# Kernel tuning notes

Hardware: AMD Instinct MI355X
Metric: run time of the kernel (lower is better)

Reference implementation:

```python
import jax, jax.numpy as jnp
import numpy as np

H = 64   # gru_hidden_dim == gnn_hidden_dim
F = 64   # node_feat_dim
K = 8    # k_nn
OUT = 32 # output_factor_dim
BN_EPS = 1e-5


def _gru_scan(x, Wih, Whh, bih, bhh):
    # x: [S, F] single sequence (torch bug makes GRU scan the b*n axis); returns [S, H]
    xp = x @ Wih.T + bih  # [S, 3H], gate order r,z,n (torch convention)
    def step(h, xt):
        hp = h @ Whh.T + bhh
        r = jax.nn.sigmoid(xt[:H] + hp[:H])
        z = jax.nn.sigmoid(xt[H:2 * H] + hp[H:2 * H])
        ng = jnp.tanh(xt[2 * H:] + r * hp[2 * H:])
        hn = (1.0 - z) * ng + z * h
        return hn, hn
    _, out = jax.lax.scan(step, jnp.zeros((H,), x.dtype), xp)
    return out


def _gcn_layer(x, row, col, w, W, b, n):
    # PyG GCNConv: out[col] += d^{-1/2}[row] * w * d^{-1/2}[col] * (x @ W.T)[row] + b
    xw = x @ W.T
    deg = jnp.zeros((n,), x.dtype).at[col].add(w)
    dinv = deg ** -0.5
    dinv = jnp.where(jnp.isinf(dinv), 0.0, dinv)
    norm = dinv[row] * w * dinv[col]
    out = jnp.zeros_like(xw).at[col].add(norm[:, None] * xw[row])
    return out + b


def setup_inputs() -> dict:
    key = jax.random.key(0)
    ks = jax.random.split(key, 20)
    s = 0.08  # ~ torch uniform(-1/sqrt(64), 1/sqrt(64)) scale
    d = {
        'x_seq': jax.random.normal(ks[0], (4, 8, F, 2048), jnp.float32),
        # gru_sim params
        'Wih_s': jax.random.normal(ks[1], (3 * H, F), jnp.float32) * s,
        'Whh_s': jax.random.normal(ks[2], (3 * H, H), jnp.float32) * s,
        'bih_s': jax.random.normal(ks[3], (3 * H,), jnp.float32) * s,
        'bhh_s': jax.random.normal(ks[4], (3 * H,), jnp.float32) * s,
        # gru params
        'Wih': jax.random.normal(ks[5], (3 * H, F), jnp.float32) * s,
        'Whh': jax.random.normal(ks[6], (3 * H, H), jnp.float32) * s,
        'bih': jax.random.normal(ks[7], (3 * H,), jnp.float32) * s,
        'bhh': jax.random.normal(ks[8], (3 * H,), jnp.float32) * s,
        # gcn1 / gcn2 params (GCNConv weight [out,in], bias [out])
        'W1': jax.random.normal(ks[9], (H, H), jnp.float32) * s,
        'b1': jnp.zeros((H,), jnp.float32),
        'W2': jax.random.normal(ks[10], (H, H), jnp.float32) * s,
        'b2': jnp.zeros((H,), jnp.float32),
        # batchnorm affine
        'gamma': jnp.ones((H,), jnp.float32),
        'beta': jnp.zeros((H,), jnp.float32),
        # predictor
        'Wp': jax.random.normal(ks[11], (OUT, H), jnp.float32) * s,
        'bp': jnp.zeros((OUT,), jnp.float32),
    }
    return d


def reference(x_seq, Wih_s, Whh_s, bih_s, bhh_s, Wih, Whh, bih, bhh,
              W1, b1, W2, b2, gamma, beta, Wp, bp):
    b, l, f, n = x_seq.shape
    # torch GRU is batch_first=True but fed [l, b*n, f]: it scans the b*n axis
    # as time and gru_out[-1] keeps only batch item l-1 -> only last time slice used.
    seq = x_seq[:, -1].transpose(0, 2, 1).reshape(b * n, f)  # [b*n, f]
    h = _gru_scan(seq, Wih_s, Whh_s, bih_s, bhh_s).reshape(b, n, H)      # gru_sim
    h_out = _gru_scan(seq, Wih, Whh, bih, bhh).reshape(b, n, H)          # gru

    # dynamic kNN graph from similarity
    sim = jnp.einsum('bni,bmi->bnm', h, h)
    eye = jnp.eye(n, dtype=bool)
    sim = jnp.where(eye[None], jnp.asarray(-1e9, sim.dtype), sim)
    vals, idx = jax.lax.top_k(sim, K)  # [b, n, K], sorted desc like torch.topk

    # edges: n*K knn edges + n unit-weight self loops (outer add_self_loops;
    # GCNConv's add_remaining_self_loops then adds nothing)
    row = jnp.concatenate([jnp.repeat(jnp.arange(n), K), jnp.arange(n)])

    def per_graph(v, ix, x):
        col = jnp.concatenate([ix.reshape(-1), jnp.arange(n)])
        w = jnp.concatenate([v.reshape(-1), jnp.ones((n,), v.dtype)])
        o1 = jax.nn.relu(_gcn_layer(x, row, col, w, W1, b1, n))
        o2 = jax.nn.relu(_gcn_layer(o1, row, col, w, W2, b2, n))
        return o2

    out2 = jax.vmap(per_graph)(vals, idx, h_out)  # [b, n, H]

    # BatchNorm1d (training mode: biased batch stats over b*n rows)
    flat = out2.reshape(b * n, H)
    mu = flat.mean(0)
    var = flat.var(0)
    normed = (flat - mu) / jnp.sqrt(var + BN_EPS) * gamma + beta

    out = normed @ Wp.T + bp
    return out.reshape(b, n, OUT)
```

## Files before the change

kernel.cpp:

```cpp
#include <hip/hip_runtime.h>
#include <hip/hip_bf16.h>

typedef __hip_bfloat16 bf16;

#define NB   4
#define NN   2048
#define NROW 8192
#define HD   64
#define G3   192
#define KNN  8
#define OUTD 32
#define SCHUNK 32
#define SBURN  96
#define NCH    256
#define SCH4   32
#define SBRN4  40
#define NCH4   256
#define TI   4
#define TOPB 256
#define XPR  32
#define SCR  32
#define TKR  16

#define OFF_FLAG  0u
#define OFF_DEG   64u
#define OFF_DINV  8256u
#define OFF_BNS   16448u
#define OFF_BNSQ  16512u
#define OFF_SCALE 16576u
#define OFF_SHIFT 16640u
#define OFF_VALS  16704u
#define OFF_IDX   82240u
#define OFF_A     147776u
#define OFF_C     672064u
#define OFF_XP0   1196352u
#define OFF_XP1   2769216u
#define OFF_END   4342080u

typedef __attribute__((ext_vector_type(8))) short short8v;
typedef __attribute__((ext_vector_type(4))) float f32x4;

__device__ __forceinline__ float sigmoidf_(float x) { return 1.f / (1.f + __expf(-x)); }
__device__ __forceinline__ float tanhf_(float x) {
    float e = __expf(-2.f * fabsf(x));
    float t = (1.f - e) / (1.f + e);
    return copysignf(t, x);
}
__device__ __forceinline__ float ld(const void* p, size_t i, int isbf) {
    return isbf ? __bfloat162float(((const bf16*)p)[i]) : ((const float*)p)[i];
}
__device__ __forceinline__ float bcast(float v, int k) {
    return __int_as_float(__builtin_amdgcn_readlane(__float_as_int(v), k));
}
__device__ __forceinline__ unsigned short bf16rne(float f) {
    unsigned u = __float_as_uint(f);
    return (unsigned short)((u + 0x7FFFu + ((u >> 16) & 1u)) >> 16);
}

__global__ void probe_kernel(const void* __restrict__ gamma, int* __restrict__ flag)
{
    unsigned w = ((const unsigned*)gamma)[0];
    *flag = (w == 0x3F800000u) ? 0 : 1;
}

__global__ __launch_bounds__(384) void xp_kernel(
    const void* __restrict__ x_seq,
    const void* __restrict__ Wih_s, const void* __restrict__ bih_s,
    const void* __restrict__ Wih,   const void* __restrict__ bih,
    float* __restrict__ xp0, float* __restrict__ xp1,
    const int* __restrict__ dtp)
{
    int isbf = *dtp;
    int row0 = blockIdx.x * XPR;
    int b = row0 >> 11, j0 = row0 & 2047;
    int t = threadIdx.x;

    __shared__ __align__(16) float S[XPR * 68];
    for (int idx = t; idx < XPR * HD; idx += 384) {
        int f = idx >> 5, jj = idx & (XPR - 1);
        S[jj * 68 + f] = ld(x_seq, (size_t)((b * 8 + 7) * 64 + f) * 2048 + (j0 + jj), isbf);
    }

    int g = t % G3;
    const void* W  = (t < G3) ? Wih_s : Wih;
    const void* bi = (t < G3) ? bih_s : bih;
    float* o = (t < G3) ? xp0 : xp1;
    float wreg[64];
    #pragma unroll
    for (int k = 0; k < 64; ++k) wreg[k] = ld(W, g * HD + k, isbf);
    float bias = ld(bi, g, isbf);
    __syncthreads();

    for (int jj = 0; jj < XPR; ++jj) {
        const float4* s4 = (const float4*)(S + jj * 68);
        float a0 = bias, a1 = 0.f, a2 = 0.f, a3 = 0.f;
        #pragma unroll
        for (int q = 0; q < 16; ++q) {
            float4 v = s4[q];
            a0 += wreg[4*q+0] * v.x;
            a1 += wreg[4*q+1] * v.y;
            a2 += wreg[4*q+2] * v.z;
            a3 += wreg[4*q+3] * v.w;
        }
        o[(size_t)(row0 + jj) * G3 + g] = (a0 + a1) + (a2 + a3);
    }
}

__global__ __launch_bounds__(64) void gru_scan_pack_kernel(
    const float* __restrict__ xp0, const float* __restrict__ xp1,
    const void* __restrict__ Whh_s, const void* __restrict__ bhh_s,
    const void* __restrict__ Whh,   const void* __restrict__ bhh,
    unsigned short* __restrict__ hAhi, unsigned short* __restrict__ hAlo,
    float* __restrict__ hC,
    const int* __restrict__ dtp)
{
    int isbf = *dtp;
    int gru   = blockIdx.x >> 8;
    int chunk = blockIdx.x & (NCH4 - 1);
    const float* xpp = gru ? xp1 : xp0;
    const void* Wh   = gru ? Whh : Whh_s;
    const void* bh_p = gru ? bhh : bhh_s;

    int L = threadIdx.x;

    __shared__ __align__(16) float4 SW4[64 * 64];

    for (int k = 0; k < 64; ++k) {
        float4 v;
        v.x = ld(Wh, (size_t)L * 64 + k, isbf);
        v.y = ld(Wh, (size_t)(64 + L) * 64 + k, isbf);
        v.z = ld(Wh, (size_t)(128 + L) * 64 + k, isbf);
        v.w = 0.f;
        SW4[k * 64 + L] = v;
    }
    float br  = ld(bh_p, L, isbf);
    float bz  = ld(bh_p, 64 + L, isbf);
    float bn_ = ld(bh_p, 128 + L, isbf);
    __syncthreads();

    int first = chunk * SCH4;
    int burn  = min(SBRN4, first);
    int start = first - burn;
    int steps = burn + SCH4;

    float hval = 0.f;
    size_t rb = (size_t)start * G3;
    float xr = xpp[rb + L];
    float xz = xpp[rb + 64 + L];
    float xn = xpp[rb + 128 + L];

    for (int t = 0; t < steps; ++t) {
        size_t nb = (size_t)min(start + t + 1, NROW - 1) * G3;
        float pxr = xpp[nb + L];
        float pxz = xpp[nb + 64 + L];
        float pxn = xpp[nb + 128 + L];

        float pr0 = br, pz0 = bz, pn0 = bn_;
        float pr1 = 0.f, pz1 = 0.f, pn1 = 0.f;
        #pragma unroll
        for (int k = 0; k < 64; k += 2) {
            float4 w0 = SW4[k * 64 + L];
            float4 w1 = SW4[(k + 1) * 64 + L];
            float b0 = bcast(hval, k);
            float b1 = bcast(hval, k + 1);
            pr0 += w0.x * b0; pz0 += w0.y * b0; pn0 += w0.z * b0;
            pr1 += w1.x * b1; pz1 += w1.y * b1; pn1 += w1.z * b1;
        }

        float r  = sigmoidf_(xr + pr0 + pr1);
        float z  = sigmoidf_(xz + pz0 + pz1);
        float ng = tanhf_(xn + r * (pn0 + pn1));
        hval = (1.f - z) * ng + z * hval;

        if (t >= burn) {
            size_t o = (size_t)(start + t) * HD + L;
            if (gru) {
                hC[o] = hval;
            } else {
                unsigned short hb = bf16rne(hval);
                float hf = __uint_as_float(((unsigned)hb) << 16);
                hAhi[o] = hb;
                hAlo[o] = bf16rne(hval - hf);
            }
        }
        xr = pxr; xz = pxz; xn = pxn;
    }
}

__global__ __launch_bounds__(192, 2) void gru_scan_fused_kernel(
    const void* __restrict__ x_seq,
    const void* __restrict__ Wih_s, const void* __restrict__ bih_s,
    const void* __restrict__ Whh_s, const void* __restrict__ bhh_s,
    const void* __restrict__ Wih,   const void* __restrict__ bih,
    const void* __restrict__ Whh,   const void* __restrict__ bhh,
    float* __restrict__ hA, float* __restrict__ hC,
    const int* __restrict__ dtp)
{
    int isbf = *dtp;
    int gru   = blockIdx.x >> 8;
    int chunk = blockIdx.x & 255;
    const void* Wh = gru ? Whh : Whh_s;
    const void* bh_p = gru ? bhh : bhh_s;
    const void* Wi = gru ? Wih : Wih_s;
    const void* bi_p = gru ? bih : bih_s;
    float* hout = gru ? hC : hA;

    int lane = threadIdx.x & 63;
    int w    = threadIdx.x >> 6;
    int g    = w * 64 + lane;

    float whh[64], wih[64];
    #pragma unroll
    for (int k = 0; k < 64; ++k) {
        whh[k] = ld(Wh, g * 64 + k, isbf);
        wih[k] = ld(Wi, g * 64 + k, isbf);
    }
    float bh = ld(bh_p, g, isbf);
    float bi = ld(bi_p, g, isbf);

    __shared__ float hs[64];
    __shared__ float ss[64];
    __shared__ float gr[64], gz[64], ga[64], gx[64];

    int first = chunk * SCHUNK;
    int burn  = min(SBURN, first);
    int start = first - burn;
    int steps = burn + SCHUNK;

    #define XIDX(r) ((size_t)((((r) >> 11) * 8 + 7) * 64 + lane) * 2048 + ((r) & 2047))
    float sf = 0.f;
    if (w == 0) {
        ss[lane] = ld(x_seq, XIDX(start), isbf);
        if (steps > 1) sf = ld(x_seq, XIDX(start + 1), isbf);
    }
    __syncthreads();

    float hval = 0.f;
    float sval = ss[lane];

    for (int t = 0; t < steps; ++t) {
        float a = bh, x = bi;
        #pragma unroll
        for (int k = 0; k < 64; ++k) {
            a += whh[k] * bcast(hval, k);
            x += wih[k] * bcast(sval, k);
        }
        if (w == 0)      gr[lane] = sigmoidf_(x + a);
        else if (w == 1) gz[lane] = sigmoidf_(x + a);
        else           { ga[lane] = a; gx[lane] = x; }
        __syncthreads();
        if (w == 0) {
            if (t + 1 < steps) {
                ss[lane] = sf;
                if (t + 2 < steps) sf = ld(x_seq, XIDX(start + t + 2), isbf);
            }
        } else if (w == 2) {
            float hn = (1.f - gz[lane]) * tanhf_(gx[lane] + gr[lane] * ga[lane])
                     + gz[lane] * hval;
            hs[lane] = hn;
            hval = hn;
            if (t >= burn) hout[(size_t)(start + t) * HD + lane] = hn;
        }
        __syncthreads();
        if (w != 2) hval = hs[lane];
        sval = ss[lane];
    }
    #undef XIDX
}

__device__ __forceinline__ void merge8(float tv[KNN], int tj[KNN], int off)
{
    float ov[KNN]; int oj[KNN];
    #pragma unroll
    for (int m = 0; m < KNN; ++m) {
        ov[m] = __shfl_xor(tv[m], off);
        oj[m] = __shfl_xor(tj[m], off);
    }
    #pragma unroll
    for (int m = 0; m < KNN; ++m) {
        if (ov[KNN - 1 - m] > tv[m]) { tv[m] = ov[KNN - 1 - m]; tj[m] = oj[KNN - 1 - m]; }
    }
    #pragma unroll
    for (int d = 4; d > 0; d >>= 1) {
        #pragma unroll
        for (int m = 0; m < KNN; ++m) {
            if ((m & d) == 0 && (m | d) < KNN) {
                int p = m | d;
                if (tv[p] > tv[m]) {
                    float fv = tv[m]; tv[m] = tv[p]; tv[p] = fv;
                    int fj = tj[m]; tj[m] = tj[p]; tj[p] = fj;
                }
            }
        }
    }
}

__global__ __launch_bounds__(256) void topk_mfma_kernel(
    const unsigned short* __restrict__ Ahi, const unsigned short* __restrict__ Alo,
    float* __restrict__ vals, int* __restrict__ idxs, float* __restrict__ deg)
{
    int bid = blockIdx.x;
    int row0 = bid * TKR;
    int bbase = row0 & ~(NN - 1);
    int rloc = row0 & (NN - 1);
    int t = threadIdx.x;
    int w = t >> 6, L = t & 63;
    int cL = L & 15, q = L >> 4;
    int chunk = q * 8;

    __shared__ __align__(16) float sw[4][64 * 20];
    __shared__ float mv[4][TKR][KNN];
    __shared__ int   mj[4][TKR][KNN];

    size_t arow = (size_t)(row0 + cL) * HD;
    short8v ahi0 = *(const short8v*)(Ahi + arow + chunk);
    short8v ahi1 = *(const short8v*)(Ahi + arow + 32 + chunk);
    short8v alo0 = *(const short8v*)(Alo + arow + chunk);
    short8v alo1 = *(const short8v*)(Alo + arow + 32 + chunk);

    int jbase = w * 512;
    float* swv = sw[w];
    int r = L >> 2, p = L & 3;

    float tv[KNN]; int tj[KNN];
    #pragma unroll
    for (int m = 0; m < KNN; ++m) { tv[m] = -3e38f; tj[m] = 0; }

    #pragma unroll 1
    for (int strip = 0; strip < 8; ++strip) {
        #pragma unroll
        for (int g = 0; g < 4; ++g) {
            int j0 = jbase + strip * 64 + g * 16;
            size_t brow = (size_t)(bbase + j0 + cL) * HD;
            short8v bhi0 = *(const short8v*)(Ahi + brow + chunk);
            short8v bhi1 = *(const short8v*)(Ahi + brow + 32 + chunk);
            short8v blo0 = *(const short8v*)(Alo + brow + chunk);
            short8v blo1 = *(const short8v*)(Alo + brow + 32 + chunk);
            f32x4 accA = {0.f, 0.f, 0.f, 0.f};
            f32x4 accB = {0.f, 0.f, 0.f, 0.f};
            accA = __builtin_amdgcn_mfma_f32_16x16x32_bf16(ahi0, bhi0, accA, 0, 0, 0);
            accB = __builtin_amdgcn_mfma_f32_16x16x32_bf16(ahi0, blo0, accB, 0, 0, 0);
            accA = __builtin_amdgcn_mfma_f32_16x16x32_bf16(ahi1, bhi1, accA, 0, 0, 0);
            accB = __builtin_amdgcn_mfma_f32_16x16x32_bf16(ahi1, blo1, accB, 0, 0, 0);
            accA = __builtin_amdgcn_mfma_f32_16x16x32_bf16(alo0, bhi0, accA, 0, 0, 0);
            accB = __builtin_amdgcn_mfma_f32_16x16x32_bf16(alo1, bhi1, accB, 0, 0, 0);
            f32x4 acc = accA + accB;
            *(f32x4*)(swv + (g * 16 + cL) * 20 + q * 4) = acc;
        }
        int cb = jbase + strip * 64;
        #pragma unroll 1
        for (int ci = 0; ci < 16; ++ci) {
            int c = (ci << 2) + p;
            float nv = swv[c * 20 + r];
            int j = cb + c;
            nv = (j == rloc + r) ? -1e9f : nv;
            if (nv > tv[KNN - 1]) {
                tv[KNN - 1] = nv; tj[KNN - 1] = j;
                #pragma unroll
                for (int m = KNN - 1; m > 0; --m) {
                    if (tv[m] > tv[m - 1]) {
                        float fv = tv[m]; tv[m] = tv[m - 1]; tv[m - 1] = fv;
                        int fj = tj[m]; tj[m] = tj[m - 1]; tj[m - 1] = fj;
                    }
                }
            }
        }
    }

    merge8(tv, tj, 1);
    merge8(tv, tj, 2);
    if (p == 0) {
        #pragma unroll
        for (int m = 0; m < KNN; ++m) { mv[w][r][m] = tv[m]; mj[w][r][m] = tj[m]; }
    }
    __syncthreads();

    if (w == 0) {
        int wv = p;
        #pragma unroll
        for (int m = 0; m < KNN; ++m) { tv[m] = mv[wv][r][m]; tj[m] = mj[wv][r][m]; }
        merge8(tv, tj, 1);
        merge8(tv, tj, 2);
        if (wv == 0) {
            int row = row0 + r;
            #pragma unroll
            for (int m = 0; m < KNN; ++m) {
                vals[(size_t)row * KNN + m] = tv[m];
                idxs[(size_t)row * KNN + m] = tj[m];
                atomicAdd(deg + bbase + tj[m], tv[m]);
            }
            atomicAdd(deg + row, 1.0f);
        }
    }
}

__global__ __launch_bounds__(TOPB, 2) void topk_kernel(
    const float* __restrict__ h,
    float* __restrict__ vals, int* __restrict__ idxs, float* __restrict__ deg)
{
    int bid = blockIdx.x;
    int b    = bid >> 9;
    int row0 = b * NN + (bid & 511) * TI;
    int i0 = row0 & 2047;
    int t = threadIdx.x;

    __shared__ __align__(16) float sim[TI][NN];
    __shared__ __align__(16) float hi[TI * HD];

    for (int q = t; q < TI * HD; q += TOPB)
        hi[q] = h[(size_t)(row0 + (q >> 6)) * HD + (q & 63)];
    __syncthreads();

    const float* hb = h + (size_t)b * NN * HD;
    const float4* hi4 = (const float4*)hi;
    #pragma unroll 1
    for (int j = t; j < NN; j += TOPB) {
        const float4* hr = (const float4*)(hb + (size_t)j * HD);
        float acc[TI];
        #pragma unroll
        for (int m = 0; m < TI; ++m) acc[m] = 0.f;
        #pragma unroll 4
        for (int q = 0; q < 16; ++q) {
            float4 v = hr[q];
            #pragma unroll
            for (int m = 0; m < TI; ++m) {
                float4 c = hi4[m * 16 + q];
                acc[m] += v.x*c.x + v.y*c.y + v.z*c.z + v.w*c.w;
            }
        }
        #pragma unroll
        for (int m = 0; m < TI; ++m)
            sim[m][j] = (j == i0 + m) ? -1e9f : acc[m];
    }
    __syncthreads();

    int w    = t >> 6;
    int lane = t & 63;
    int row  = row0 + w;

    float tv[KNN]; int tj[KNN];
    #pragma unroll
    for (int m = 0; m < KNN; ++m) { tv[m] = -3e38f; tj[m] = 0; }

    for (int k = 0; k < 32; ++k) {
        int j = lane + (k << 6);
        float nv = sim[w][j];
        if (nv > tv[KNN - 1]) {
            tv[KNN - 1] = nv; tj[KNN - 1] = j;
            #pragma unroll
            for (int m = KNN - 1; m > 0; --m) {
                if (tv[m] > tv[m - 1]) {
                    float fv = tv[m]; tv[m] = tv[m - 1]; tv[m - 1] = fv;
                    int fj = tj[m]; tj[m] = tj[m - 1]; tj[m - 1] = fj;
                }
            }
        }
    }

    #pragma unroll
    for (int off = 1; off < 64; off <<= 1) {
        float ov[KNN]; int oj[KNN];
        #pragma unroll
        for (int m = 0; m < KNN; ++m) {
            ov[m] = __shfl_xor(tv[m], off);
            oj[m] = __shfl_xor(tj[m], off);
        }
        #pragma unroll
        for (int m = 0; m < KNN; ++m) {
            if (ov[KNN - 1 - m] > tv[m]) { tv[m] = ov[KNN - 1 - m]; tj[m] = oj[KNN - 1 - m]; }
        }
        if (off < 32) {
            #pragma unroll
            for (int d = 4; d > 0; d >>= 1) {
                #pragma unroll
                for (int m = 0; m < KNN; ++m) {
                    if ((m & d) == 0 && (m | d) < KNN) {
                        int p = m | d;
                        if (tv[p] > tv[m]) {
                            float fv = tv[m]; tv[m] = tv[p]; tv[p] = fv;
                            int fj = tj[m]; tj[m] = tj[p]; tj[p] = fj;
                        }
                    }
                }
            }
        }
    }

    if (lane == 0) {
        #pragma unroll
        for (int m = 0; m < KNN; ++m) {
            vals[(size_t)row * KNN + m] = tv[m];
            idxs[(size_t)row * KNN + m] = tj[m];
            atomicAdd(deg + (b << 11) + tj[m], tv[m]);
        }
        atomicAdd(deg + row, 1.0f);
    }
}

__global__ void dinv_kernel(const float* __restrict__ deg, float* __restrict__ dinv)
{
    int g = blockIdx.x * 256 + threadIdx.x;
    if (g >= NROW) return;
    float d = deg[g];
    float r = 1.f / sqrtf(d);
    dinv[g] = isinf(r) ? 0.f : r;
}

__global__ __launch_bounds__(256) void scatter_kernel(
    const float* __restrict__ in, const void* __restrict__ W,
    const void* __restrict__ bias, int dorelu,
    const float* __restrict__ dinv,
    const float* __restrict__ vals, const int* __restrict__ idxs,
    float* __restrict__ acc, const int* __restrict__ dtp)
{
    int isbf = *dtp;
    int lane = threadIdx.x & 63;
    int w    = threadIdx.x >> 6;

    float wreg[64];
    #pragma unroll
    for (int k = 0; k < 64; ++k) wreg[k] = ld(W, lane * HD + k, isbf);
    float bb = ld(bias, lane, isbf);

    int row0 = blockIdx.x * SCR + w * (SCR / 4);
    #pragma unroll 1
    for (int rr = 0; rr < SCR / 4; ++rr) {
        int row = row0 + rr;
        int b = row >> 11;
        float x = in[(size_t)row * HD + lane];
        if (dorelu) x = fmaxf(x + bb, 0.f);
        float v0 = 0.f, v1 = 0.f, v2 = 0.f, v3 = 0.f;
        #pragma unroll
        for (int k = 0; k < 64; k += 4) {
            v0 += wreg[k]     * bcast(x, k);
            v1 += wreg[k + 1] * bcast(x, k + 1);
            v2 += wreg[k + 2] * bcast(x, k + 2);
            v3 += wreg[k + 3] * bcast(x, k + 3);
        }
        float v = (v0 + v1) + (v2 + v3);
        float di = dinv[row];
        atomicAdd(acc + (size_t)row * HD + lane, di * di * v);
        #pragma unroll
        for (int k = 0; k < KNN; ++k) {
            int c = idxs[(size_t)row * KNN + k];
            float wv = vals[(size_t)row * KNN + k];
            float nw = di * wv * dinv[(b << 11) + c];
            atomicAdd(acc + (size_t)((b << 11) + c) * HD + lane, nw * v);
        }
    }
}

__global__ void bn_stats_kernel(const float* __restrict__ acc2, const void* __restrict__ bias,
                                float* __restrict__ bns, float* __restrict__ bnsq,
                                const int* __restrict__ dtp)
{
    int isbf = *dtp;
    int c = blockIdx.x;
    int t = threadIdx.x;
    float bb = ld(bias, c, isbf);
    float s = 0.f, s2 = 0.f;
    for (int r = t; r < NROW; r += 256) {
        float v = fmaxf(acc2[(size_t)r * HD + c] + bb, 0.f);
        s += v; s2 += v * v;
    }
    __shared__ float sv[4], sv2[4];
    #pragma unroll
    for (int off = 32; off > 0; off >>= 1) {
        s  += __shfl_down(s, off);
        s2 += __shfl_down(s2, off);
    }
    if ((t & 63) == 0) { sv[t >> 6] = s; sv2[t >> 6] = s2; }
    __syncthreads();
    if (t == 0) {
        for (int w = 1; w < 4; ++w) { s += sv[w]; s2 += sv2[w]; }
        bns[c] = s; bnsq[c] = s2;
    }
}

__global__ void bn_final_kernel(const float* __restrict__ bns, const float* __restrict__ bnsq,
                                const void* __restrict__ gamma, const void* __restrict__ beta,
                                float* __restrict__ scale, float* __restrict__ shift,
                                const int* __restrict__ dtp)
{
    int isbf = *dtp;
    int c = threadIdx.x;
    float mu = bns[c] / (float)NROW;
    float var = fmaxf(bnsq[c] / (float)NROW - mu * mu, 0.f);
    float sc = ld(gamma, c, isbf) / sqrtf(var + 1e-5f);
    scale[c] = sc;
    shift[c] = ld(beta, c, isbf) - mu * sc;
}

__global__ void out_kernel(const float* __restrict__ acc2, const void* __restrict__ bias2,
                           const float* __restrict__ scale, const float* __restrict__ shift,
                           const void* __restrict__ Wp, const void* __restrict__ bp,
                           float* __restrict__ out, const int* __restrict__ dtp)
{
    int isbf = *dtp;
    int row0 = blockIdx.x * 2;
    int t = threadIdx.x;
    __shared__ float nl[2 * HD];
    for (int q = t; q < 2 * HD; q += 64) {
        int r = q >> 6, c = q & (HD - 1);
        float v = fmaxf(acc2[(size_t)(row0 + r) * HD + c] + ld(bias2, c, isbf), 0.f);
        nl[q] = v * scale[c] + shift[c];
    }
    __syncthreads();
    int rr = t >> 5, o = t & 31;
    float acc = ld(bp, o, isbf);
    #pragma unroll
    for (int k = 0; k < HD; ++k) acc += nl[rr * HD + k] * ld(Wp, o * HD + k, isbf);
    out[(size_t)(row0 + rr) * OUTD + o] = acc;
}

extern "C" void kernel_launch(void* const* d_in, const int* in_sizes, int n_in,
                              void* d_out, int out_size, void* d_ws, size_t ws_size,
                              hipStream_t stream)
{
    (void)in_sizes; (void)n_in; (void)out_size;
    const void* x_seq = d_in[0];
    const void* Wih_s = d_in[1];
    const void* Whh_s = d_in[2];
    const void* bih_s = d_in[3];
    const void* bhh_s = d_in[4];
    const void* Wih   = d_in[5];
    const void* Whh   = d_in[6];
    const void* bih   = d_in[7];
    const void* bhh   = d_in[8];
    const void* W1    = d_in[9];
    const void* b1    = d_in[10];
    const void* W2    = d_in[11];
    const void* b2    = d_in[12];
    const void* gamma = d_in[13];
    const void* beta  = d_in[14];
    const void* Wp    = d_in[15];
    const void* bp    = d_in[16];
    float* out = (float*)d_out;

    float* ws = (float*)d_ws;
    int*   dtp  = (int*)(ws + OFF_FLAG);
    float* deg  = ws + OFF_DEG;
    float* dinv = ws + OFF_DINV;
    float* bns  = ws + OFF_BNS;
    float* bnsq = ws + OFF_BNSQ;
    float* scale = ws + OFF_SCALE;
    float* shift = ws + OFF_SHIFT;
    float* vals = ws + OFF_VALS;
    int*   idxs = (int*)(ws + OFF_IDX);
    float* A    = ws + OFF_A;
    float* C    = ws + OFF_C;
    float* xp0  = ws + OFF_XP0;
    float* xp1  = ws + OFF_XP1;

    bool big_ws = ws_size >= (size_t)OFF_END * sizeof(float);

    probe_kernel<<<1, 1, 0, stream>>>(gamma, dtp);
    hipMemsetAsync(deg, 0, NROW * sizeof(float), stream);

    if (big_ws) {
        xp_kernel<<<NROW / XPR, 384, 0, stream>>>(x_seq, Wih_s, bih_s, Wih, bih, xp0, xp1, dtp);
        gru_scan_pack_kernel<<<2 * NCH4, 64, 0, stream>>>(
            xp0, xp1, Whh_s, bhh_s, Whh, bhh,
            (unsigned short*)A, (unsigned short*)A + (size_t)NROW * HD, C, dtp);
        topk_mfma_kernel<<<NROW / TKR, 256, 0, stream>>>(
            (unsigned short*)A, (unsigned short*)A + (size_t)NROW * HD, vals, idxs, deg);
    } else {
        gru_scan_fused_kernel<<<2 * NCH, 192, 0, stream>>>(x_seq, Wih_s, bih_s, Whh_s, bhh_s,
                                                           Wih, bih, Whh, bhh, A, C, dtp);
        topk_kernel<<<NROW / TI, TOPB, 0, stream>>>(A, vals, idxs, deg);
    }
    dinv_kernel<<<NROW / 256, 256, 0, stream>>>(deg, dinv);

    hipMemsetAsync(A, 0, (size_t)NROW * HD * sizeof(float), stream);
    scatter_kernel<<<NROW / SCR, 256, 0, stream>>>(C, W1, b1, 0, dinv, vals, idxs, A, dtp);

    hipMemsetAsync(C, 0, (size_t)NROW * HD * sizeof(float), stream);
    scatter_kernel<<<NROW / SCR, 256, 0, stream>>>(A, W2, b1, 1, dinv, vals, idxs, C, dtp);

    bn_stats_kernel<<<HD, 256, 0, stream>>>(C, b2, bns, bnsq, dtp);
    bn_final_kernel<<<1, HD, 0, stream>>>(bns, bnsq, gamma, beta, scale, shift, dtp);
    out_kernel<<<NROW / 2, 64, 0, stream>>>(C, b2, scale, shift, Wp, bp, out, dtp);
}
```

Baseline: 383.8 us.

## Keep per-lane top-k lists on MFMA accumulators in registers, drop LDS staging

The kNN top-k kernel no longer writes each 16x16 MFMA tile to shared memory and rereads it. Each lane now keeps four independent top-8 insertion lists, one per accumulator element (row), fed directly from the accumulator. The lists are then combined with a 4-step cross-lane merge over the 16 lanes that share a row. This removes LDS stores, loads and address math. In exchange it quadruples the register-held sorting state (64 values), which may raise register pressure and cut occupancy, and it runs 16 merge8 shuffle rounds per lane instead of 2.

After: 372.2 us. 1.03x faster.

```diff
diff --git a/kernel.cpp b/kernel.cpp
--- a/kernel.cpp
+++ b/kernel.cpp
@@ -308,7 +308,6 @@
     int cL = L & 15, q = L >> 4;
     int chunk = q * 8;
 
-    __shared__ __align__(16) float sw[4][64 * 20];
     __shared__ float mv[4][TKR][KNN];
     __shared__ int   mj[4][TKR][KNN];
 
@@ -319,12 +318,12 @@
     short8v alo1 = *(const short8v*)(Alo + arow + 32 + chunk);
 
     int jbase = w * 512;
-    float* swv = sw[w];
-    int r = L >> 2, p = L & 3;
-
-    float tv[KNN]; int tj[KNN];
-    #pragma unroll
-    for (int m = 0; m < KNN; ++m) { tv[m] = -3e38f; tj[m] = 0; }
+
+    float tv[4][KNN]; int tj[4][KNN];
+    #pragma unroll
+    for (int e = 0; e < 4; ++e)
+        #pragma unroll
+        for (int m = 0; m < KNN; ++m) { tv[e][m] = -3e38f; tj[e][m] = 0; }
 
     #pragma unroll 1
     for (int strip = 0; strip < 8; ++strip) {
@@ -345,49 +344,57 @@
             accA = __builtin_amdgcn_mfma_f32_16x16x32_bf16(alo0, bhi0, accA, 0, 0, 0);
             accB = __builtin_amdgcn_mfma_f32_16x16x32_bf16(alo1, bhi1, accB, 0, 0, 0);
             f32x4 acc = accA + accB;
-            *(f32x4*)(swv + (g * 16 + cL) * 20 + q * 4) = acc;
-        }
-        int cb = jbase + strip * 64;
-        #pragma unroll 1
-        for (int ci = 0; ci < 16; ++ci) {
-            int c = (ci << 2) + p;
-            float nv = swv[c * 20 + r];
-            int j = cb + c;
-            nv = (j == rloc + r) ? -1e9f : nv;
-            if (nv > tv[KNN - 1]) {
-                tv[KNN - 1] = nv; tj[KNN - 1] = j;
-                #pragma unroll
-                for (int m = KNN - 1; m > 0; --m) {
-                    if (tv[m] > tv[m - 1]) {
-                        float fv = tv[m]; tv[m] = tv[m - 1]; tv[m - 1] = fv;
-                        int fj = tj[m]; tj[m] = tj[m - 1]; tj[m - 1] = fj;
+            int jj = j0 + cL;
+            #pragma unroll
+            for (int e = 0; e < 4; ++e) {
+                int r = q * 4 + e;
+                float nv = (jj == rloc + r) ? -1e9f : acc[e];
+                if (nv > tv[e][KNN - 1]) {
+                    tv[e][KNN - 1] = nv; tj[e][KNN - 1] = jj;
+                    #pragma unroll
+                    for (int m = KNN - 1; m > 0; --m) {
+                        if (tv[e][m] > tv[e][m - 1]) {
+                            float fv = tv[e][m]; tv[e][m] = tv[e][m - 1]; tv[e][m - 1] = fv;
+                            int fj = tj[e][m]; tj[e][m] = tj[e][m - 1]; tj[e][m - 1] = fj;
+                        }
                     }
                 }
             }
         }
     }
 
-    merge8(tv, tj, 1);
-    merge8(tv, tj, 2);
-    if (p == 0) {
-        #pragma unroll
-        for (int m = 0; m < KNN; ++m) { mv[w][r][m] = tv[m]; mj[w][r][m] = tj[m]; }
+    #pragma unroll
+    for (int e = 0; e < 4; ++e) {
+        merge8(tv[e], tj[e], 1);
+        merge8(tv[e], tj[e], 2);
+        merge8(tv[e], tj[e], 4);
+        merge8(tv[e], tj[e], 8);
+    }
+    if (cL == 0) {
+        #pragma unroll
+        for (int e = 0; e < 4; ++e)
+            #pragma unroll
+            for (int m = 0; m < KNN; ++m) {
+                mv[w][q * 4 + e][m] = tv[e][m];
+                mj[w][q * 4 + e][m] = tj[e][m];
+            }
     }
     __syncthreads();
 
     if (w == 0) {
-        int wv = p;
-        #pragma unroll
-        for (int m = 0; m < KNN; ++m) { tv[m] = mv[wv][r][m]; tj[m] = mj[wv][r][m]; }
-        merge8(tv, tj, 1);
-        merge8(tv, tj, 2);
-        if (wv == 0) {
+        int r = L >> 2, p = L & 3;
+        float fv[KNN]; int fj[KNN];
+        #pragma unroll
+        for (int m = 0; m < KNN; ++m) { fv[m] = mv[p][r][m]; fj[m] = mj[p][r][m]; }
+        merge8(fv, fj, 1);
+        merge8(fv, fj, 2);
+        if (p == 0) {
             int row = row0 + r;
             #pragma unroll
             for (int m = 0; m < KNN; ++m) {
-                vals[(size_t)row * KNN + m] = tv[m];
-                idxs[(size_t)row * KNN + m] = tj[m];
-                atomicAdd(deg + bbase + tj[m], tv[m]);
+                vals[(size_t)row * KNN + m] = fv[m];
+                idxs[(size_t)row * KNN + m] = fj[m];
+                atomicAdd(deg + bbase + fj[m], fv[m]);
             }
             atomicAdd(deg + row, 1.0f);
         }
```
